# Performance work log

Measured on AMD Instinct MI355X. Metric: run time of the kernel, lower is better.

Reference implementation:

```python
import jax, jax.numpy as jnp
import numpy as np

DIM = 128
NUM_HEADS = 2
HEAD_DIM = DIM // NUM_HEADS
SCALE = HEAD_DIM ** -0.5
SR = 4
EPS_LN = 1e-5


def token2map(x, idx_token, H, W, H_init, W_init):
    """Scatter tokens x[B,N,Cc] into a [B,Cc,H,W] map via the init grid.
    Matches the sparse-COO branch of the torch token2map (N_init < N*H*W).
    """
    B, N, Cc = x.shape
    N_init = H_init * W_init
    # nearest-neighbor index of each init-grid cell in the HxW map
    rows = (jnp.arange(H_init) * H) // H_init          # floor(i * H / H_init)
    cols = (jnp.arange(W_init) * W) // W_init
    idx_hw = (rows[:, None] * W + cols[None, :]).reshape(-1)      # [N_init]
    flat = (idx_hw[None, :] + jnp.arange(B)[:, None] * (H * W)).reshape(-1)  # [B*N_init]
    # per-pixel count (A @ ones) + 1e-6, as in torch
    count = jax.ops.segment_sum(jnp.ones((B * N_init,), jnp.float32), flat,
                                num_segments=B * H * W) + 1e-6    # [B*H*W]
    gathered = jnp.take_along_axis(x, idx_token[..., None], axis=1)  # [B,N_init,Cc]
    out = jax.ops.segment_sum(gathered.reshape(B * N_init, Cc), flat,
                              num_segments=B * H * W)
    out = out / count[:, None]
    return out.reshape(B, H, W, Cc).transpose(0, 3, 1, 2)  # [B,Cc,H,W]


def setup_inputs() -> dict:
    key = jax.random.key(0)
    ks = jax.random.split(key, 12)
    B, Nq, Nkv, C = 8, 12544, 12544, DIM
    H, W, H_init, W_init = 112, 112, 224, 224
    inp = {
        'q_x': jax.random.normal(ks[0], (B, Nq, C), jnp.float32),
        'kv_x': jax.random.normal(ks[1], (B, Nkv, C), jnp.float32),
        'token_score': jax.random.normal(ks[2], (B, Nkv, 1), jnp.float32),
        'idx_token': jax.random.randint(ks[3], (B, H_init * W_init), 0, Nkv),
        'H': H, 'W': W, 'H_init': H_init, 'W_init': W_init,
        # learned params (qkv_bias=False)
        'q_w': jax.random.normal(ks[4], (C, C), jnp.float32) * 0.02,
        'kv_w': jax.random.normal(ks[5], (C, 2 * C), jnp.float32) * 0.02,
        'proj_w': jax.random.normal(ks[6], (C, C), jnp.float32) * 0.02,
        'proj_b': jnp.zeros((C,), jnp.float32),
        'sr_w': jax.random.normal(ks[7], (C, C, SR, SR), jnp.float32) * np.sqrt(2.0 / (SR * SR * C)),
        'sr_b': jnp.zeros((C,), jnp.float32),
        'norm_g': jnp.ones((C,), jnp.float32),
        'norm_b': jnp.zeros((C,), jnp.float32),
    }
    return inp


def reference(q_x, kv_x, token_score, q_w, kv_w, proj_w, proj_b, sr_w, sr_b,
              norm_g, norm_b, idx_token, H, W, H_init, W_init):
    B, Nq, C = q_x.shape
    # q projection -> [B, h, Nq, d]
    q = (q_x @ q_w).reshape(B, Nq, NUM_HEADS, HEAD_DIM).transpose(0, 2, 1, 3)

    # sr_ratio > 1 path: scatter kv tokens (with conf channel) to q's map
    tmp = jnp.concatenate([kv_x, token_score], axis=-1)          # [B,Nkv,C+1]
    tmp_map = token2map(tmp, idx_token, H, W, H_init, W_init)    # [B,C+1,H,W]
    kv_map = tmp_map[:, :C]                                      # [B,C,H,W]
    conf_map = tmp_map[:, C:]                                    # [B,1,H,W]

    # spatial reduction conv (kernel=stride=SR) + LayerNorm
    kv_r = jax.lax.conv_general_dilated(
        kv_map, sr_w, window_strides=(SR, SR), padding='VALID',
        dimension_numbers=('NCHW', 'OIHW', 'NCHW')) + sr_b[None, :, None, None]
    h, w = kv_r.shape[2], kv_r.shape[3]
    Ns = h * w
    kv_t = kv_r.reshape(B, C, Ns).transpose(0, 2, 1)             # [B,Ns,C]
    mu = jnp.mean(kv_t, axis=-1, keepdims=True)
    var = jnp.mean(jnp.square(kv_t - mu), axis=-1, keepdims=True)
    kv_t = (kv_t - mu) / jnp.sqrt(var + EPS_LN) * norm_g + norm_b

    # avg-pool conf to the reduced grid
    conf = conf_map.reshape(B, 1, h, SR, w, SR).mean(axis=(3, 5)).reshape(B, Ns)

    # kv projection -> k,v [B,h,Ns,d]
    kv_p = (kv_t @ kv_w).reshape(B, Ns, 2, NUM_HEADS, HEAD_DIM).transpose(2, 0, 3, 1, 4)
    k, v = kv_p[0], kv_p[1]

    attn = jnp.einsum('bhqd,bhkd->bhqk', q * SCALE, k) + conf[:, None, None, :]
    attn = jax.nn.softmax(attn, axis=-1)
    out = jnp.einsum('bhqk,bhkd->bhqd', attn, v).transpose(0, 2, 1, 3).reshape(B, Nq, C)
    return out @ proj_w + proj_b
```

## Files before the change

### kernel.cpp

```cpp
#include <hip/hip_runtime.h>
#include <hip/hip_bf16.h>


#define NBATCH 8
#define NQTOK  12544
#define NSP    832
#define LOG2E  1.4426950408889634f
#define QSCALE (0.125f * LOG2E)

typedef __attribute__((ext_vector_type(8))) short bf8;
typedef __attribute__((ext_vector_type(4))) float f4;
typedef __attribute__((ext_vector_type(4))) unsigned short u16x4;
typedef __attribute__((ext_vector_type(2))) unsigned int u32x2;

#define MFMA16(a, b, c) __builtin_amdgcn_mfma_f32_16x16x32_bf16((a), (b), (c), 0, 0, 0)

#if __has_builtin(__builtin_amdgcn_exp2f)
#define EXP2(x) __builtin_amdgcn_exp2f(x)
#else
#define EXP2(x) exp2f(x)
#endif

__device__ __forceinline__ unsigned short f2b(float x) {
  union { float f; unsigned u; } v; v.f = x;
  unsigned r = v.u + 0x7FFFu + ((v.u >> 16) & 1u);
  return (unsigned short)(r >> 16);
}

__device__ __forceinline__ unsigned pk2(float lo, float hi) {
  float2 t; t.x = lo; t.y = hi;
  __hip_bfloat162 bb = __float22bfloat162_rn(t);
  union { __hip_bfloat162 b; unsigned u; } v; v.b = bb;
  return v.u;
}

__device__ __forceinline__ bf8 ldfrag(const unsigned short* t, int stride, int rbase, int kbase) {
  int lane = threadIdx.x & 63;
  return *(const bf8*)(t + (rbase + (lane & 15)) * stride + kbase + ((lane >> 4) << 3));
}

__global__ void k_setup(const float* __restrict__ qw, const float* __restrict__ kvw,
                        const float* __restrict__ pw, const float* __restrict__ srw,
                        unsigned short* __restrict__ qwt, unsigned short* __restrict__ kvwt,
                        unsigned short* __restrict__ pwt, unsigned short* __restrict__ srwt,
                        unsigned* __restrict__ kb, unsigned* __restrict__ vb,
                        float* __restrict__ conf) {
  int tid = blockIdx.x * 256 + threadIdx.x;
  int nt = gridDim.x * 256;
  for (int i = tid; i < 128 * 128; i += nt) {
    int k = i >> 7, n = i & 127;
    qwt[n * 128 + k] = f2b(qw[k * 128 + n]);
    pwt[n * 128 + k] = f2b(pw[k * 128 + n]);
  }
  for (int i = tid; i < 128 * 256; i += nt) {
    int k = i >> 8, j = i & 255;
    kvwt[j * 128 + k] = f2b(kvw[k * 256 + j]);
  }
  for (int i = tid; i < 128 * 2048; i += nt) {
    int o = i >> 11, kk = i & 2047;
    int p = kk >> 7, c = kk & 127;
    srwt[o * 2048 + kk] = f2b(srw[o * 2048 + c * 16 + p]);
  }
  const int nu = NBATCH * 2 * NSP * 64 / 2;
  for (int i = tid; i < nu; i += nt) { kb[i] = 0u; vb[i] = 0u; }
  for (int i = tid; i < NBATCH * NSP; i += nt) conf[i] = -1e30f;
}

__global__ void k_token2map(const float* __restrict__ kv_x, const float* __restrict__ tsc,
                            const int* __restrict__ idxt,
                            unsigned short* __restrict__ kv_map, float* __restrict__ conf_map) {
  int half = threadIdx.x >> 7;
  int c = threadIdx.x & 127;
  int cell = blockIdx.x * 2 + half;
  int b = cell / 12544, hw = cell - b * 12544;
  int h = hw / 112, w = hw - h * 112;
  const int* it = idxt + b * 50176;
  int t0 = it[(2 * h) * 224 + 2 * w];
  int t1 = it[(2 * h) * 224 + 2 * w + 1];
  int t2 = it[(2 * h + 1) * 224 + 2 * w];
  int t3 = it[(2 * h + 1) * 224 + 2 * w + 1];
  const float* base = kv_x + (long)b * 12544 * 128;
  const float recip = 1.0f / (4.0f + 1e-6f);
  float s = base[t0 * 128 + c] + base[t1 * 128 + c] + base[t2 * 128 + c] + base[t3 * 128 + c];
  kv_map[(long)cell * 128 + c] = f2b(s * recip);
  if (c == 0) {
    const float* ts = tsc + b * 12544;
    conf_map[cell] = (ts[t0] + ts[t1] + ts[t2] + ts[t3]) * recip;
  }
}

__launch_bounds__(256)
__global__ void k_conv_ln(const unsigned short* __restrict__ kv_map,
                          const unsigned short* __restrict__ srwt,
                          const float* __restrict__ srb, const float* __restrict__ ng,
                          const float* __restrict__ nb, unsigned short* __restrict__ kv_t,
                          const float* __restrict__ conf_map, float* __restrict__ conf) {
  __shared__ unsigned short At[64 * 136];
  __shared__ unsigned short Bt[128 * 136];
  const int tid = threadIdx.x;
  const int lane = tid & 63, w = tid >> 6;
  const int l15 = lane & 15, g = lane >> 4;
  const int r0 = blockIdx.x * 64;
  if (tid < 64) {
    int pos = r0 + tid;
    int bq = pos / 784, p2 = pos - bq * 784;
    int oh = p2 / 28, ow = p2 - oh * 28;
    float s = 0.f;
#pragma unroll
    for (int kh = 0; kh < 4; kh++)
#pragma unroll
      for (int kw = 0; kw < 4; kw++)
        s += conf_map[bq * 12544 + (4 * oh + kh) * 112 + 4 * ow + kw];
    conf[bq * NSP + p2] = s * (LOG2E / 16.0f);
  }
  const f4 fz = {0.f, 0.f, 0.f, 0.f};
  f4 acc[8];
#pragma unroll
  for (int i = 0; i < 8; i++) acc[i] = fz;

  for (int p = 0; p < 16; p++) {
#pragma unroll
    for (int j = 0; j < 4; j++) {
      int id = tid + 256 * j;
      int row = id >> 4, c0 = (id & 15) << 3;
      int rr = r0 + row;
      int bb = rr / 784, pos = rr - bb * 784;
      int oh = pos / 28, ow = pos - oh * 28;
      long src = ((long)(bb * 12544 + (4 * oh + (p >> 2)) * 112 + 4 * ow + (p & 3))) * 128 + c0;
      *(uint4*)(At + row * 136 + c0) = *(const uint4*)(kv_map + src);
    }
#pragma unroll
    for (int j = 0; j < 8; j++) {
      int id = tid + 256 * j;
      int row = id >> 4, c0 = (id & 15) << 3;
      *(uint4*)(Bt + row * 136 + c0) = *(const uint4*)(srwt + row * 2048 + p * 128 + c0);
    }
    __syncthreads();
#pragma unroll
    for (int ks = 0; ks < 4; ks++) {
      bf8 a = ldfrag(At, 136, 16 * w, 32 * ks);
#pragma unroll
      for (int nf = 0; nf < 8; nf++) {
        bf8 bb = ldfrag(Bt, 136, 16 * nf, 32 * ks);
        acc[nf] = MFMA16(a, bb, acc[nf]);
      }
    }
    __syncthreads();
  }
  float sum_[4] = {0.f, 0.f, 0.f, 0.f}, sq_[4] = {0.f, 0.f, 0.f, 0.f};
#pragma unroll
  for (int nf = 0; nf < 8; nf++) {
    float bias = srb[16 * nf + l15];
#pragma unroll
    for (int reg = 0; reg < 4; reg++) {
      float v = acc[nf][reg] + bias;
      acc[nf][reg] = v;
      sum_[reg] += v;
      sq_[reg] += v * v;
    }
  }
#pragma unroll
  for (int msk = 1; msk < 16; msk <<= 1)
#pragma unroll
    for (int reg = 0; reg < 4; reg++) {
      sum_[reg] += __shfl_xor(sum_[reg], msk, 64);
      sq_[reg] += __shfl_xor(sq_[reg], msk, 64);
    }
  float mean[4], rstd[4];
#pragma unroll
  for (int reg = 0; reg < 4; reg++) {
    mean[reg] = sum_[reg] * (1.0f / 128.0f);
    float var = sq_[reg] * (1.0f / 128.0f) - mean[reg] * mean[reg];
    rstd[reg] = rsqrtf(var + 1e-5f);
  }
#pragma unroll
  for (int nf = 0; nf < 8; nf++) {
    float gc = ng[16 * nf + l15], bc = nb[16 * nf + l15];
#pragma unroll
    for (int reg = 0; reg < 4; reg++) {
      int row = r0 + 16 * w + 4 * g + reg;
      float v = (acc[nf][reg] - mean[reg]) * rstd[reg] * gc + bc;
      kv_t[row * 128 + 16 * nf + l15] = f2b(v);
    }
  }
}

__launch_bounds__(256)
__global__ void k_kv(const unsigned short* __restrict__ kv_t,
                     const unsigned short* __restrict__ kvwt,
                     unsigned short* __restrict__ kbuf, unsigned short* __restrict__ vbuf) {
  __shared__ unsigned short At[64 * 136];
  __shared__ unsigned short Bt[128 * 136];
  const int tid = threadIdx.x;
  const int lane = tid & 63, w = tid >> 6;
  const int l15 = lane & 15, g = lane >> 4;
  const int r0 = blockIdx.x * 64;
  const int sel = blockIdx.y;
#pragma unroll
  for (int j = 0; j < 4; j++) {
    int id = tid + 256 * j;
    int row = id >> 4, c0 = (id & 15) << 3;
    *(uint4*)(At + row * 136 + c0) = *(const uint4*)(kv_t + (long)(r0 + row) * 128 + c0);
  }
#pragma unroll
  for (int j = 0; j < 8; j++) {
    int id = tid + 256 * j;
    int row = id >> 4, c0 = (id & 15) << 3;
    *(uint4*)(Bt + row * 136 + c0) = *(const uint4*)(kvwt + (long)(sel * 128 + row) * 128 + c0);
  }
  __syncthreads();
  const f4 fz = {0.f, 0.f, 0.f, 0.f};
  f4 acc[8];
#pragma unroll
  for (int i = 0; i < 8; i++) acc[i] = fz;
#pragma unroll
  for (int ks = 0; ks < 4; ks++) {
    bf8 a = ldfrag(At, 136, 16 * w, 32 * ks);
#pragma unroll
    for (int nf = 0; nf < 8; nf++) {
      bf8 bb = ldfrag(Bt, 136, 16 * nf, 32 * ks);
      acc[nf] = MFMA16(a, bb, acc[nf]);
    }
  }
#pragma unroll
  for (int nf = 0; nf < 8; nf++)
#pragma unroll
    for (int reg = 0; reg < 4; reg++) {
      int r = r0 + 16 * w + 4 * g + reg;
      int b = r / 784, ns = r - b * 784;
      int j = 16 * nf + l15;
      int hh = j >> 6, d = j & 63;
      unsigned short val = f2b(acc[nf][reg]);
      if (sel == 0) kbuf[((long)(b * 2 + hh) * NSP + ns) * 64 + d] = val;
      else          vbuf[((long)(b * 2 + hh) * 64 + d) * NSP + ns] = val;
    }
}

__launch_bounds__(256)
__global__ void k_q(const float* __restrict__ q_x, const unsigned short* __restrict__ qwt,
                    unsigned short* __restrict__ qbuf) {
  __shared__ unsigned short At[64 * 136];
  __shared__ unsigned short Bt[128 * 136];
  const int tid = threadIdx.x;
  const int lane = tid & 63, w = tid >> 6;
  const int l15 = lane & 15, g = lane >> 4;
  const int r0 = blockIdx.x * 64;
#pragma unroll
  for (int j = 0; j < 8; j++) {
    int id = tid + 256 * j;
    int row = id >> 5, c0 = (id & 31) << 2;
    float4 v = *(const float4*)(q_x + (long)(r0 + row) * 128 + c0);
    u16x4 o;
    o[0] = f2b(v.x); o[1] = f2b(v.y); o[2] = f2b(v.z); o[3] = f2b(v.w);
    *(u16x4*)(At + row * 136 + c0) = o;
  }
#pragma unroll
  for (int j = 0; j < 8; j++) {
    int id = tid + 256 * j;
    int row = id >> 4, c0 = (id & 15) << 3;
    *(uint4*)(Bt + row * 136 + c0) = *(const uint4*)(qwt + (long)row * 128 + c0);
  }
  __syncthreads();
  const f4 fz = {0.f, 0.f, 0.f, 0.f};
  f4 acc[8];
#pragma unroll
  for (int i = 0; i < 8; i++) acc[i] = fz;
#pragma unroll
  for (int ks = 0; ks < 4; ks++) {
    bf8 a = ldfrag(At, 136, 16 * w, 32 * ks);
#pragma unroll
    for (int nf = 0; nf < 8; nf++) {
      bf8 bb = ldfrag(Bt, 136, 16 * nf, 32 * ks);
      acc[nf] = MFMA16(a, bb, acc[nf]);
    }
  }
#pragma unroll
  for (int nf = 0; nf < 8; nf++)
#pragma unroll
    for (int reg = 0; reg < 4; reg++) {
      int r = r0 + 16 * w + 4 * g + reg;
      int b = r / NQTOK, n = r - b * NQTOK;
      int j = 16 * nf + l15;
      int hh = j >> 6, d = j & 63;
      qbuf[((long)(b * 2 + hh) * NQTOK + n) * 64 + d] = f2b(acc[nf][reg] * QSCALE);
    }
}

__launch_bounds__(256, 3)
__global__ void k_attn(const unsigned short* __restrict__ qbuf,
                       const unsigned short* __restrict__ kbuf,
                       const unsigned short* __restrict__ vbuf,
                       const float* __restrict__ conf,
                       unsigned short* __restrict__ attbuf) {
  __shared__ unsigned short Kt[2][64 * 72];
  __shared__ unsigned short Vt[2][64 * 72];
  const int tid = threadIdx.x;
  const int lane = tid & 63, w = tid >> 6;
  const int l15 = lane & 15, g = lane >> 4;
  const int h = blockIdx.y, b = blockIdx.z;
  const int bh = b * 2 + h;
  const int q0 = blockIdx.x * 128 + 32 * w;

  const unsigned short* qsrc = qbuf + ((long)bh * NQTOK + q0) * 64;
  bf8 qf[2][2];
#pragma unroll
  for (int mr = 0; mr < 2; mr++)
#pragma unroll
    for (int ks = 0; ks < 2; ks++)
      qf[mr][ks] = *(const bf8*)(qsrc + (16 * mr + l15) * 64 + 32 * ks + (g << 3));

  const int srow = tid >> 2;
  const int scol = (tid & 3) << 4;
  const unsigned short* kg = kbuf + (long)bh * NSP * 64 + srow * 64 + scol;
  const unsigned short* vg = vbuf + (long)bh * 64 * NSP + (long)srow * NSP + scol;
  unsigned short* klds = &Kt[0][0] + srow * 72 + scol;
  unsigned short* vlds = &Vt[0][0] + srow * 72 + scol;

  uint4 kr0, kr1, vr0, vr1;
#define ISSUE(T)                                                   \
  do {                                                             \
    const unsigned short* kp_ = kg + (long)(T) * 4096;             \
    const unsigned short* vp_ = vg + (T) * 64;                     \
    kr0 = *(const uint4*)(kp_);                                    \
    kr1 = *(const uint4*)(kp_ + 8);                                \
    vr0 = *(const uint4*)(vp_);                                    \
    vr1 = *(const uint4*)(vp_ + 8);                                \
  } while (0)
#define STWRITE(BUF)                                               \
  do {                                                             \
    unsigned short* kd_ = klds + (BUF) * 4608;                     \
    unsigned short* vd_ = vlds + (BUF) * 4608;                     \
    *(uint4*)kd_ = kr0;  *(uint4*)(kd_ + 8) = kr1;                 \
    *(uint4*)vd_ = vr0;  *(uint4*)(vd_ + 8) = vr1;                 \
  } while (0)

  ISSUE(0);
  STWRITE(0);
  ISSUE(1);
  __syncthreads();

  const f4 fz = {0.f, 0.f, 0.f, 0.f};
  f4 ao[2][4], aol[2];
#pragma unroll
  for (int mr = 0; mr < 2; mr++) {
    aol[mr] = fz;
#pragma unroll
    for (int i = 0; i < 4; i++) ao[mr][i] = fz;
  }
  const short on = (short)0x3F80;
  const bf8 onesf = {on, on, on, on, on, on, on, on};
  const float* confb = conf + b * NSP;

#pragma unroll 2
  for (int t = 0; t < 13; t++) {
    const int cur = t & 1;
    const unsigned short* KtB = &Kt[cur][0];
    const unsigned short* VtB = &Vt[cur][0];
    bf8 kf[4][2];
#pragma unroll
    for (int mf = 0; mf < 4; mf++)
#pragma unroll
      for (int ks = 0; ks < 2; ks++)
        kf[mf][ks] = ldfrag(KtB, 72, 16 * mf, 32 * ks);
    bf8 vf[4][2];
#pragma unroll
    for (int nfd = 0; nfd < 4; nfd++)
#pragma unroll
      for (int ks = 0; ks < 2; ks++)
        vf[nfd][ks] = ldfrag(VtB, 72, 16 * nfd, 32 * ks);
    float4 cv[4];
#pragma unroll
    for (int mf = 0; mf < 4; mf++)
      cv[mf] = *(const float4*)(confb + t * 64 + 16 * mf + 4 * g);
#pragma unroll
    for (int mr = 0; mr < 2; mr++) {
      f4 s_[4];
#pragma unroll
      for (int mf = 0; mf < 4; mf++) s_[mf] = fz;
#pragma unroll
      for (int ks = 0; ks < 2; ks++)
#pragma unroll
        for (int mf = 0; mf < 4; mf++)
          s_[mf] = MFMA16(kf[mf][ks], qf[mr][ks], s_[mf]);
      unsigned W[4][2];
#pragma unroll
      for (int mf = 0; mf < 4; mf++) {
        float p0 = EXP2(s_[mf][0] + cv[mf].x);
        float p1 = EXP2(s_[mf][1] + cv[mf].y);
        float p2 = EXP2(s_[mf][2] + cv[mf].z);
        float p3 = EXP2(s_[mf][3] + cv[mf].w);
        W[mf][0] = pk2(p0, p1);
        W[mf][1] = pk2(p2, p3);
      }
#pragma unroll
      for (int ks = 0; ks < 2; ks++) {
        u32x2 r0 = __builtin_amdgcn_permlane32_swap(W[2 * ks][0], W[2 * ks + 1][0], false, false);
        u32x2 t02 = __builtin_amdgcn_permlane16_swap(r0.x, r0.y, false, false);
        u32x2 r1 = __builtin_amdgcn_permlane32_swap(W[2 * ks][1], W[2 * ks + 1][1], false, false);
        u32x2 t13 = __builtin_amdgcn_permlane16_swap(r1.x, r1.y, false, false);
        union { unsigned u[4]; bf8 v; } pa;
        pa.u[0] = t02.x; pa.u[1] = t13.x; pa.u[2] = t02.y; pa.u[3] = t13.y;
        aol[mr] = MFMA16(pa.v, onesf, aol[mr]);
#pragma unroll
        for (int nfd = 0; nfd < 4; nfd++)
          ao[mr][nfd] = MFMA16(pa.v, vf[nfd][ks], ao[mr][nfd]);
      }
    }
    if (t < 12) STWRITE(cur ^ 1);
    if (t < 11) ISSUE(t + 2);
    __syncthreads();
  }
#undef ISSUE
#undef STWRITE
#pragma unroll
  for (int mr = 0; mr < 2; mr++) {
    float inv[4];
#pragma unroll
    for (int reg = 0; reg < 4; reg++) inv[reg] = 1.0f / aol[mr][reg];
#pragma unroll
    for (int nfd = 0; nfd < 4; nfd++)
#pragma unroll
      for (int reg = 0; reg < 4; reg++) {
        int n = q0 + 16 * mr + 4 * g + reg;
        int col = h * 64 + 16 * nfd + l15;
        attbuf[((long)b * NQTOK + n) * 128 + col] = f2b(ao[mr][nfd][reg] * inv[reg]);
      }
  }
}

__launch_bounds__(256)
__global__ void k_proj(const unsigned short* __restrict__ attbuf,
                       const unsigned short* __restrict__ pwt,
                       const float* __restrict__ pb, float* __restrict__ out) {
  __shared__ unsigned short At[64 * 136];
  __shared__ unsigned short Bt[128 * 136];
  const int tid = threadIdx.x;
  const int lane = tid & 63, w = tid >> 6;
  const int l15 = lane & 15, g = lane >> 4;
  const int r0 = blockIdx.x * 64;
#pragma unroll
  for (int j = 0; j < 4; j++) {
    int id = tid + 256 * j;
    int row = id >> 4, c0 = (id & 15) << 3;
    *(uint4*)(At + row * 136 + c0) = *(const uint4*)(attbuf + (long)(r0 + row) * 128 + c0);
  }
#pragma unroll
  for (int j = 0; j < 8; j++) {
    int id = tid + 256 * j;
    int row = id >> 4, c0 = (id & 15) << 3;
    *(uint4*)(Bt + row * 136 + c0) = *(const uint4*)(pwt + (long)row * 128 + c0);
  }
  __syncthreads();
  const f4 fz = {0.f, 0.f, 0.f, 0.f};
  f4 acc[8];
#pragma unroll
  for (int i = 0; i < 8; i++) acc[i] = fz;
#pragma unroll
  for (int ks = 0; ks < 4; ks++) {
    bf8 a = ldfrag(At, 136, 16 * w, 32 * ks);
#pragma unroll
    for (int nf = 0; nf < 8; nf++) {
      bf8 bb = ldfrag(Bt, 136, 16 * nf, 32 * ks);
      acc[nf] = MFMA16(a, bb, acc[nf]);
    }
  }
#pragma unroll
  for (int nf = 0; nf < 8; nf++) {
    float bias = pb[16 * nf + l15];
#pragma unroll
    for (int reg = 0; reg < 4; reg++) {
      int r = r0 + 16 * w + 4 * g + reg;
      out[(long)r * 128 + 16 * nf + l15] = acc[nf][reg] + bias;
    }
  }
}

extern "C" void kernel_launch(void* const* d_in, const int* in_sizes, int n_in,
                              void* d_out, int out_size, void* d_ws, size_t ws_size,
                              hipStream_t stream) {
  const float* q_x  = (const float*)d_in[0];
  const float* kv_x = (const float*)d_in[1];
  const float* tsc  = (const float*)d_in[2];
  const int*   idxt = (const int*)d_in[3];
  const float* q_w  = (const float*)d_in[8];
  const float* kv_w = (const float*)d_in[9];
  const float* pw   = (const float*)d_in[10];
  const float* pb   = (const float*)d_in[11];
  const float* srw  = (const float*)d_in[12];
  const float* srb  = (const float*)d_in[13];
  const float* ng   = (const float*)d_in[14];
  const float* nb   = (const float*)d_in[15];
  float* outp = (float*)d_out;

  char* ws = (char*)d_ws;
  size_t off = 0;
  auto take = [&](size_t bytes) {
    char* p = ws + off;
    off += (bytes + 255) & ~(size_t)255;
    return p;
  };
  unsigned short* qwt   = (unsigned short*)take(128 * 128 * 2);
  unsigned short* pwt   = (unsigned short*)take(128 * 128 * 2);
  unsigned short* kvwt  = (unsigned short*)take(256 * 128 * 2);
  unsigned short* srwt  = (unsigned short*)take(128 * 2048 * 2);
  unsigned short* kvmap = (unsigned short*)take((size_t)NBATCH * 12544 * 128 * 2);
  float* conf_map       = (float*)take((size_t)NBATCH * 12544 * 4);
  unsigned short* kvt   = (unsigned short*)take((size_t)NBATCH * 784 * 128 * 2);
  unsigned short* kbuf  = (unsigned short*)take((size_t)NBATCH * 2 * NSP * 64 * 2);
  unsigned short* vbuf  = (unsigned short*)take((size_t)NBATCH * 2 * NSP * 64 * 2);
  float* conf           = (float*)take((size_t)NBATCH * NSP * 4);
  unsigned short* qbuf  = (unsigned short*)take((size_t)NBATCH * 2 * NQTOK * 64 * 2);
  unsigned short* attbuf = kvmap;

  k_setup<<<512, 256, 0, stream>>>(q_w, kv_w, pw, srw, qwt, kvwt, pwt, srwt,
                                   (unsigned*)kbuf, (unsigned*)vbuf, conf);
  k_token2map<<<50176, 256, 0, stream>>>(kv_x, tsc, idxt, kvmap, conf_map);
  k_conv_ln<<<98, 256, 0, stream>>>(kvmap, srwt, srb, ng, nb, kvt, conf_map, conf);
  k_kv<<<dim3(98, 2), 256, 0, stream>>>(kvt, kvwt, kbuf, vbuf);
  k_q<<<1568, 256, 0, stream>>>(q_x, qwt, qbuf);
  k_attn<<<dim3(98, 2, 8), 256, 0, stream>>>(qbuf, kbuf, vbuf, conf, attbuf);
  k_proj<<<1568, 256, 0, stream>>>(attbuf, pwt, pb, outp);
}
```

Before: 178.4 us.

## Fuse Q projection into attention kernel and vectorize token2map gather

Removes the separate k_q kernel. The attention kernel now loads its 128 q_x rows into shared memory, computes Q for its head with MFMA (with the softmax scale folded into the bf16 weight during setup), and turns the result into register fragments using permlane swaps. This avoids writing and re-reading the qbuf intermediate and saves a launch. The cost is that each (batch, head) block converts q_x and repeats the projection work for both heads, which doubles q_x reads. Separately, token2map now uses float4 loads with 8 cells per block.

```diff
diff --git a/kernel.cpp b/kernel.cpp
--- a/kernel.cpp
+++ b/kernel.cpp
@@ -32,6 +32,16 @@
   __hip_bfloat162 bb = __float22bfloat162_rn(t);
   union { __hip_bfloat162 b; unsigned u; } v; v.b = bb;
   return v.u;
+}
+
+__device__ __forceinline__ bf8 rows2frag(const unsigned W0[2], const unsigned W1[2]) {
+  u32x2 r0 = __builtin_amdgcn_permlane32_swap(W0[0], W1[0], false, false);
+  u32x2 t02 = __builtin_amdgcn_permlane16_swap(r0.x, r0.y, false, false);
+  u32x2 r1 = __builtin_amdgcn_permlane32_swap(W0[1], W1[1], false, false);
+  u32x2 t13 = __builtin_amdgcn_permlane16_swap(r1.x, r1.y, false, false);
+  union { unsigned u[4]; bf8 v; } pa;
+  pa.u[0] = t02.x; pa.u[1] = t13.x; pa.u[2] = t02.y; pa.u[3] = t13.y;
+  return pa.v;
 }
 
 __device__ __forceinline__ bf8 ldfrag(const unsigned short* t, int stride, int rbase, int kbase) {
@@ -49,7 +59,7 @@
   int nt = gridDim.x * 256;
   for (int i = tid; i < 128 * 128; i += nt) {
     int k = i >> 7, n = i & 127;
-    qwt[n * 128 + k] = f2b(qw[k * 128 + n]);
+    qwt[n * 128 + k] = f2b(qw[k * 128 + n] * QSCALE);
     pwt[n * 128 + k] = f2b(pw[k * 128 + n]);
   }
   for (int i = tid; i < 128 * 256; i += nt) {
@@ -69,9 +79,9 @@
 __global__ void k_token2map(const float* __restrict__ kv_x, const float* __restrict__ tsc,
                             const int* __restrict__ idxt,
                             unsigned short* __restrict__ kv_map, float* __restrict__ conf_map) {
-  int half = threadIdx.x >> 7;
-  int c = threadIdx.x & 127;
-  int cell = blockIdx.x * 2 + half;
+  int tid = threadIdx.x;
+  int cell = blockIdx.x * 8 + (tid >> 5);
+  int c0 = (tid & 31) << 2;
   int b = cell / 12544, hw = cell - b * 12544;
   int h = hw / 112, w = hw - h * 112;
   const int* it = idxt + b * 50176;
@@ -79,11 +89,19 @@
   int t1 = it[(2 * h) * 224 + 2 * w + 1];
   int t2 = it[(2 * h + 1) * 224 + 2 * w];
   int t3 = it[(2 * h + 1) * 224 + 2 * w + 1];
-  const float* base = kv_x + (long)b * 12544 * 128;
+  const float* base = kv_x + (long)b * 12544 * 128 + c0;
   const float recip = 1.0f / (4.0f + 1e-6f);
-  float s = base[t0 * 128 + c] + base[t1 * 128 + c] + base[t2 * 128 + c] + base[t3 * 128 + c];
-  kv_map[(long)cell * 128 + c] = f2b(s * recip);
-  if (c == 0) {
+  float4 a0 = *(const float4*)(base + (long)t0 * 128);
+  float4 a1 = *(const float4*)(base + (long)t1 * 128);
+  float4 a2 = *(const float4*)(base + (long)t2 * 128);
+  float4 a3 = *(const float4*)(base + (long)t3 * 128);
+  u16x4 o;
+  o[0] = f2b((a0.x + a1.x + a2.x + a3.x) * recip);
+  o[1] = f2b((a0.y + a1.y + a2.y + a3.y) * recip);
+  o[2] = f2b((a0.z + a1.z + a2.z + a3.z) * recip);
+  o[3] = f2b((a0.w + a1.w + a2.w + a3.w) * recip);
+  *(u16x4*)(kv_map + (long)cell * 128 + c0) = o;
+  if ((tid & 31) == 0) {
     const float* ts = tsc + b * 12544;
     conf_map[cell] = (ts[t0] + ts[t1] + ts[t2] + ts[t3]) * recip;
   }
@@ -236,85 +254,71 @@
     }
 }
 
-__launch_bounds__(256)
-__global__ void k_q(const float* __restrict__ q_x, const unsigned short* __restrict__ qwt,
-                    unsigned short* __restrict__ qbuf) {
-  __shared__ unsigned short At[64 * 136];
-  __shared__ unsigned short Bt[128 * 136];
-  const int tid = threadIdx.x;
-  const int lane = tid & 63, w = tid >> 6;
-  const int l15 = lane & 15, g = lane >> 4;
-  const int r0 = blockIdx.x * 64;
-#pragma unroll
-  for (int j = 0; j < 8; j++) {
-    int id = tid + 256 * j;
-    int row = id >> 5, c0 = (id & 31) << 2;
-    float4 v = *(const float4*)(q_x + (long)(r0 + row) * 128 + c0);
-    u16x4 o;
-    o[0] = f2b(v.x); o[1] = f2b(v.y); o[2] = f2b(v.z); o[3] = f2b(v.w);
-    *(u16x4*)(At + row * 136 + c0) = o;
-  }
-#pragma unroll
-  for (int j = 0; j < 8; j++) {
-    int id = tid + 256 * j;
-    int row = id >> 4, c0 = (id & 15) << 3;
-    *(uint4*)(Bt + row * 136 + c0) = *(const uint4*)(qwt + (long)row * 128 + c0);
-  }
-  __syncthreads();
-  const f4 fz = {0.f, 0.f, 0.f, 0.f};
-  f4 acc[8];
-#pragma unroll
-  for (int i = 0; i < 8; i++) acc[i] = fz;
-#pragma unroll
-  for (int ks = 0; ks < 4; ks++) {
-    bf8 a = ldfrag(At, 136, 16 * w, 32 * ks);
-#pragma unroll
-    for (int nf = 0; nf < 8; nf++) {
-      bf8 bb = ldfrag(Bt, 136, 16 * nf, 32 * ks);
-      acc[nf] = MFMA16(a, bb, acc[nf]);
-    }
-  }
-#pragma unroll
-  for (int nf = 0; nf < 8; nf++)
-#pragma unroll
-    for (int reg = 0; reg < 4; reg++) {
-      int r = r0 + 16 * w + 4 * g + reg;
-      int b = r / NQTOK, n = r - b * NQTOK;
-      int j = 16 * nf + l15;
-      int hh = j >> 6, d = j & 63;
-      qbuf[((long)(b * 2 + hh) * NQTOK + n) * 64 + d] = f2b(acc[nf][reg] * QSCALE);
-    }
-}
-
 __launch_bounds__(256, 3)
-__global__ void k_attn(const unsigned short* __restrict__ qbuf,
+__global__ void k_attn(const float* __restrict__ q_x,
+                       const unsigned short* __restrict__ qwt,
                        const unsigned short* __restrict__ kbuf,
                        const unsigned short* __restrict__ vbuf,
                        const float* __restrict__ conf,
                        unsigned short* __restrict__ attbuf) {
-  __shared__ unsigned short Kt[2][64 * 72];
-  __shared__ unsigned short Vt[2][64 * 72];
+  __shared__ unsigned short SMEM[18432];
   const int tid = threadIdx.x;
   const int lane = tid & 63, w = tid >> 6;
   const int l15 = lane & 15, g = lane >> 4;
   const int h = blockIdx.y, b = blockIdx.z;
   const int bh = b * 2 + h;
-  const int q0 = blockIdx.x * 128 + 32 * w;
-
-  const unsigned short* qsrc = qbuf + ((long)bh * NQTOK + q0) * 64;
+  const int q0b = blockIdx.x * 128;
+  const int q0 = q0b + 32 * w;
+
+  {
+    int row = tid >> 1, ch = (tid & 1) << 6;
+    const float* src = q_x + ((long)b * NQTOK + q0b + row) * 128 + ch;
+    unsigned short* dst = SMEM + row * 136 + ch;
+#pragma unroll
+    for (int j = 0; j < 8; j++) {
+      float4 v0 = *(const float4*)(src + 8 * j);
+      float4 v1 = *(const float4*)(src + 8 * j + 4);
+      unsigned u[4];
+      u[0] = pk2(v0.x, v0.y); u[1] = pk2(v0.z, v0.w);
+      u[2] = pk2(v1.x, v1.y); u[3] = pk2(v1.z, v1.w);
+      *(uint4*)(dst + 8 * j) = *(uint4*)u;
+    }
+  }
+  __syncthreads();
   bf8 qf[2][2];
 #pragma unroll
-  for (int mr = 0; mr < 2; mr++)
-#pragma unroll
-    for (int ks = 0; ks < 2; ks++)
-      qf[mr][ks] = *(const bf8*)(qsrc + (16 * mr + l15) * 64 + 32 * ks + (g << 3));
+  for (int mr = 0; mr < 2; mr++) {
+    f4 qacc[4];
+    const f4 fz0 = {0.f, 0.f, 0.f, 0.f};
+#pragma unroll
+    for (int mf = 0; mf < 4; mf++) qacc[mf] = fz0;
+#pragma unroll
+    for (int ks4 = 0; ks4 < 4; ks4++) {
+      bf8 bqx = ldfrag(SMEM, 136, 32 * w + 16 * mr, 32 * ks4);
+#pragma unroll
+      for (int mf = 0; mf < 4; mf++) {
+        bf8 aqw = *(const bf8*)(qwt + (64 * h + 16 * mf + l15) * 128 + 32 * ks4 + (g << 3));
+        qacc[mf] = MFMA16(aqw, bqx, qacc[mf]);
+      }
+    }
+    unsigned W[4][2];
+#pragma unroll
+    for (int mf = 0; mf < 4; mf++) {
+      W[mf][0] = pk2(qacc[mf][0], qacc[mf][1]);
+      W[mf][1] = pk2(qacc[mf][2], qacc[mf][3]);
+    }
+#pragma unroll
+    for (int kap = 0; kap < 2; kap++)
+      qf[mr][kap] = rows2frag(W[2 * kap], W[2 * kap + 1]);
+  }
+  __syncthreads();
 
   const int srow = tid >> 2;
   const int scol = (tid & 3) << 4;
   const unsigned short* kg = kbuf + (long)bh * NSP * 64 + srow * 64 + scol;
   const unsigned short* vg = vbuf + (long)bh * 64 * NSP + (long)srow * NSP + scol;
-  unsigned short* klds = &Kt[0][0] + srow * 72 + scol;
-  unsigned short* vlds = &Vt[0][0] + srow * 72 + scol;
+  unsigned short* klds = SMEM + srow * 72 + scol;
+  unsigned short* vlds = SMEM + 9216 + srow * 72 + scol;
 
   uint4 kr0, kr1, vr0, vr1;
 #define ISSUE(T)                                                   \
@@ -354,8 +358,8 @@
 #pragma unroll 2
   for (int t = 0; t < 13; t++) {
     const int cur = t & 1;
-    const unsigned short* KtB = &Kt[cur][0];
-    const unsigned short* VtB = &Vt[cur][0];
+    const unsigned short* KtB = SMEM + cur * 4608;
+    const unsigned short* VtB = SMEM + 9216 + cur * 4608;
     bf8 kf[4][2];
 #pragma unroll
     for (int mf = 0; mf < 4; mf++)
@@ -394,16 +398,11 @@
       }
 #pragma unroll
       for (int ks = 0; ks < 2; ks++) {
-        u32x2 r0 = __builtin_amdgcn_permlane32_swap(W[2 * ks][0], W[2 * ks + 1][0], false, false);
-        u32x2 t02 = __builtin_amdgcn_permlane16_swap(r0.x, r0.y, false, false);
-        u32x2 r1 = __builtin_amdgcn_permlane32_swap(W[2 * ks][1], W[2 * ks + 1][1], false, false);
-        u32x2 t13 = __builtin_amdgcn_permlane16_swap(r1.x, r1.y, false, false);
-        union { unsigned u[4]; bf8 v; } pa;
-        pa.u[0] = t02.x; pa.u[1] = t13.x; pa.u[2] = t02.y; pa.u[3] = t13.y;
-        aol[mr] = MFMA16(pa.v, onesf, aol[mr]);
+        bf8 pa = rows2frag(W[2 * ks], W[2 * ks + 1]);
+        aol[mr] = MFMA16(pa, onesf, aol[mr]);
 #pragma unroll
         for (int nfd = 0; nfd < 4; nfd++)
-          ao[mr][nfd] = MFMA16(pa.v, vf[nfd][ks], ao[mr][nfd]);
+          ao[mr][nfd] = MFMA16(pa, vf[nfd][ks], ao[mr][nfd]);
       }
     }
     if (t < 12) STWRITE(cur ^ 1);
@@ -509,15 +508,13 @@
   unsigned short* kbuf  = (unsigned short*)take((size_t)NBATCH * 2 * NSP * 64 * 2);
   unsigned short* vbuf  = (unsigned short*)take((size_t)NBATCH * 2 * NSP * 64 * 2);
   float* conf           = (float*)take((size_t)NBATCH * NSP * 4);
-  unsigned short* qbuf  = (unsigned short*)take((size_t)NBATCH * 2 * NQTOK * 64 * 2);
   unsigned short* attbuf = kvmap;
 
   k_setup<<<512, 256, 0, stream>>>(q_w, kv_w, pw, srw, qwt, kvwt, pwt, srwt,
                                    (unsigned*)kbuf, (unsigned*)vbuf, conf);
-  k_token2map<<<50176, 256, 0, stream>>>(kv_x, tsc, idxt, kvmap, conf_map);
+  k_token2map<<<12544, 256, 0, stream>>>(kv_x, tsc, idxt, kvmap, conf_map);
   k_conv_ln<<<98, 256, 0, stream>>>(kvmap, srwt, srb, ng, nb, kvt, conf_map, conf);
   k_kv<<<dim3(98, 2), 256, 0, stream>>>(kvt, kvwt, kbuf, vbuf);
-  k_q<<<1568, 256, 0, stream>>>(q_x, qwt, qbuf);
-  k_attn<<<dim3(98, 2, 8), 256, 0, stream>>>(qbuf, kbuf, vbuf, conf, attbuf);
+  k_attn<<<dim3(98, 2, 8), 256, 0, stream>>>(q_x, qwt, kbuf, vbuf, conf, attbuf);
   k_proj<<<1568, 256, 0, stream>>>(attbuf, pwt, pb, outp);
 }
```

Result: no change. 179.3 us (+0.5%).
